# Kernel optimization log

Hardware: AMD Instinct MI355X
Metric: run time of the kernel (lower is better)

## Reference

```python
import jax, jax.numpy as jnp
import numpy as np

N, E, F, H, D, B = 50000, 800000, 128, 4, 32, 8  # nodes, edges, feat, heads, head_dim, graphs
NEG_SLOPE = 0.2


def _layer_norm(x, g, b, eps=1e-5):
    mu = jnp.mean(x, axis=-1, keepdims=True)
    var = jnp.var(x, axis=-1, keepdims=True)
    return (x - mu) * jax.lax.rsqrt(var + eps) * g + b


def _gat(x, src, dst, W, a_src, a_dst, bias):
    # PyG GATConv (eval): linear -> per-node alpha terms -> edge logits ->
    # per-destination segment softmax -> scatter-add weighted messages.
    h = (x @ W).reshape(N, H, D)                                  # [N,H,D]
    al_s = jnp.einsum('nhd,hd->nh', h, a_src)                     # [N,H]
    al_d = jnp.einsum('nhd,hd->nh', h, a_dst)                     # [N,H]
    logits = jax.nn.leaky_relu(al_s[src] + al_d[dst], NEG_SLOPE)  # [E+N,H]
    m = jax.ops.segment_max(logits, dst, num_segments=N)          # [N,H]
    ex = jnp.exp(logits - m[dst])
    denom = jax.ops.segment_sum(ex, dst, num_segments=N)          # [N,H]
    alpha = ex / denom[dst]                                       # [E+N,H]
    msg = h[src] * alpha[..., None]                               # [E+N,H,D]
    out = jax.ops.segment_sum(msg, dst, num_segments=N)           # [N,H,D]
    return out.reshape(N, H * D) + bias


def _gat_block(x, src, dst, W, a_src, a_dst, bias, ln_g, ln_b):
    out = _gat(x, src, dst, W, a_src, a_dst, bias)
    return _layer_norm(out + x, ln_g, ln_b)  # residual: dims match (128==128)


def setup_inputs() -> dict:
    key = jax.random.key(0)
    ks = jax.random.split(key, 24)
    s = 0.05
    inp = {
        'x': jax.random.normal(ks[0], (N, F), jnp.float32),
        'edge_index': jax.random.randint(ks[1], (2, E), 0, N, jnp.int32),
        'batch': jnp.sort(jax.random.randint(ks[2], (N,), 0, B, jnp.int32)),
    }
    i = 3
    for p in ('loc', 'reg'):
        inp[p + '_W'] = jax.random.normal(ks[i], (F, H * D)) * s; i += 1
        inp[p + '_att_src'] = jax.random.normal(ks[i], (H, D)) * s; i += 1
        inp[p + '_att_dst'] = jax.random.normal(ks[i], (H, D)) * s; i += 1
        inp[p + '_bias'] = jnp.zeros((H * D,))
        inp[p + '_ln_g'] = jnp.ones((F,))
        inp[p + '_ln_b'] = jnp.zeros((F,))
    inp['gp_W1'] = jax.random.normal(ks[i], (F, F)) * s; i += 1
    inp['gp_b1'] = jnp.zeros((F,))
    inp['gp_W2'] = jax.random.normal(ks[i], (F, F)) * s; i += 1
    inp['gp_b2'] = jnp.zeros((F,))
    inp['fu_W1'] = jax.random.normal(ks[i], (3 * F, 2 * F)) * s; i += 1
    inp['fu_b1'] = jnp.zeros((2 * F,))
    inp['fu_W2'] = jax.random.normal(ks[i], (2 * F, F)) * s; i += 1
    inp['fu_b2'] = jnp.zeros((F,))
    inp['fu_ln_g'] = jnp.ones((F,))
    inp['fu_ln_b'] = jnp.zeros((F,))
    return inp


def reference(x, edge_index, batch,
              loc_W, loc_att_src, loc_att_dst, loc_bias, loc_ln_g, loc_ln_b,
              reg_W, reg_att_src, reg_att_dst, reg_bias, reg_ln_g, reg_ln_b,
              gp_W1, gp_b1, gp_W2, gp_b2,
              fu_W1, fu_b1, fu_W2, fu_b2, fu_ln_g, fu_ln_b):
    # add self-loops (PyG GATConv default add_self_loops=True)
    loops = jnp.arange(N, dtype=edge_index.dtype)
    src = jnp.concatenate([edge_index[0], loops])
    dst = jnp.concatenate([edge_index[1], loops])

    local = _gat_block(x, src, dst, loc_W, loc_att_src, loc_att_dst, loc_bias, loc_ln_g, loc_ln_b)
    regional = _gat_block(x, src, dst, reg_W, reg_att_src, reg_att_dst, reg_bias, reg_ln_g, reg_ln_b)

    # global mean pool per graph, broadcast back to nodes
    sums = jax.ops.segment_sum(x, batch, num_segments=B)                  # [B,F]
    cnts = jax.ops.segment_sum(jnp.ones((N, 1), x.dtype), batch, num_segments=B)
    gctx = (sums / cnts)[batch]                                           # [N,F]
    gfeat = jax.nn.relu(gctx @ gp_W1 + gp_b1) @ gp_W2 + gp_b2

    cat = jnp.concatenate([local, regional, gfeat], axis=-1)              # [N,3F]
    fused = jax.nn.relu(cat @ fu_W1 + fu_b1) @ fu_W2 + fu_b2
    return _layer_norm(fused, fu_ln_g, fu_ln_b)
```

## Files before the change

kernel.cpp:

```cpp
#include <hip/hip_runtime.h>

#define NN 50000
#define EE 800000
#define FF 128
#define HH 4
#define BB 8
#define NEG 0.2f
#define NBLK ((NN + 255) / 256)

typedef __attribute__((ext_vector_type(8))) short s8v;
typedef __attribute__((ext_vector_type(4))) float f4v;

__device__ __forceinline__ unsigned short f2b(float f) {
    union { float f; unsigned u; } v; v.f = f;
    unsigned r = v.u + 0x7fffu + ((v.u >> 16) & 1u);
    return (unsigned short)(r >> 16);
}
__device__ __forceinline__ float b2f(unsigned short h) {
    union { unsigned u; float f; } v; v.u = ((unsigned)h) << 16;
    return v.f;
}
__device__ __forceinline__ float uasf(unsigned u) {
    union { unsigned u; float f; } v; v.u = u; return v.f;
}
__device__ __forceinline__ float lrelu(float t) { return t > 0.f ? t : NEG * t; }
__device__ __forceinline__ s8v cvt8(const float* p) {
    float4 f0 = *(const float4*)p;
    float4 f1 = *(const float4*)(p + 4);
    unsigned short u[8] = { f2b(f0.x), f2b(f0.y), f2b(f0.z), f2b(f0.w),
                            f2b(f1.x), f2b(f1.y), f2b(f1.z), f2b(f1.w) };
    return *(const s8v*)u;
}

__global__ void k_prep(const float* __restrict__ locW, const float* __restrict__ regW,
                       const float* __restrict__ W1, const float* __restrict__ W2,
                       unsigned short* __restrict__ Wt, unsigned short* __restrict__ W1t,
                       unsigned short* __restrict__ W2t, int* cur, float* pooled) {
    int i = blockIdx.x * 256 + threadIdx.x;
    if (i < 32768) {
        int n = i >> 7, k = i & 127;
        float v = n < 128 ? locW[k * 128 + n] : regW[k * 128 + n - 128];
        Wt[i] = f2b(v);
    } else if (i < 131072) {
        int j = i - 32768; int n = j / 384, k = j - n * 384;
        W1t[j] = f2b(W1[k * 256 + n]);
    } else if (i < 163840) {
        int j = i - 131072; int n = j >> 8, k = j & 255;
        W2t[j] = f2b(W2[k * 128 + n]);
    } else {
        int j = i - 163840;
        if (j < NN) cur[j] = 1;
        if (j < BB * FF) pooled[j] = 0.f;
    }
}

__global__ void k_count(const int* __restrict__ ei, int* cur) {
    int i = blockIdx.x * 256 + threadIdx.x;
    if (i < EE) atomicAdd(&cur[ei[EE + i]], 1);
}

__global__ __launch_bounds__(256) void k_scanA(int* cur, int* row_ptr, int* bsum) {
    __shared__ int wsum[4];
    int b = blockIdx.x, t = threadIdx.x;
    int i = b * 256 + t;
    int v = (i < NN) ? cur[i] : 0;
    if (i < NN) cur[i] = 0;
    int lane = t & 63, w = t >> 6;
    int sc = v;
#pragma unroll
    for (int off = 1; off < 64; off <<= 1) {
        int n = __shfl_up(sc, off);
        if (lane >= off) sc += n;
    }
    if (lane == 63) wsum[w] = sc;
    __syncthreads();
    int woff = 0;
    for (int k = 0; k < w; k++) woff += wsum[k];
    int incl = sc + woff;
    if (i < NN) row_ptr[i + 1] = incl;
    if (t == 255) bsum[b] = incl;
    if (i == 0) row_ptr[0] = 0;
}

__global__ __launch_bounds__(256) void k_scanC(int* row_ptr, const int* __restrict__ bsum) {
    __shared__ int ssum[4];
    int b = blockIdx.x, t = threadIdx.x;
    int lane = t & 63, w = t >> 6;
    int v = (t < b) ? bsum[t] : 0;
#pragma unroll
    for (int off = 32; off; off >>= 1) v += __shfl_xor(v, off);
    if (lane == 0) ssum[w] = v;
    __syncthreads();
    int off = ssum[0] + ssum[1] + ssum[2] + ssum[3];
    int i = b * 256 + t;
    if (i < NN && b > 0) row_ptr[i + 1] += off;
}

__global__ void k_scatter(const int* __restrict__ ei, const int* __restrict__ row_ptr,
                          int* cur, int* col) {
    int i = blockIdx.x * 256 + threadIdx.x;
    if (i < EE) {
        int s = ei[i], d = ei[EE + i];
        int p = atomicAdd(&cur[d], 1);
        col[row_ptr[d] + p] = s;
    } else if (i < EE + NN) {
        int n = i - EE;
        int p = atomicAdd(&cur[n], 1);
        col[row_ptr[n] + p] = n;
    }
}

__global__ __launch_bounds__(256) void k_gemm1(
    const float* __restrict__ x, const int* __restrict__ batch,
    const unsigned short* __restrict__ Wt,
    const float* __restrict__ loc_as, const float* __restrict__ loc_ad,
    const float* __restrict__ reg_as, const float* __restrict__ reg_ad,
    unsigned short* __restrict__ hl, unsigned short* __restrict__ hr,
    float* __restrict__ alc_s, float* __restrict__ alc_d,
    float* __restrict__ pooled) {
    __shared__ __align__(16) unsigned short SA[2][2048];
    __shared__ __align__(16) unsigned short SB[2][8192];
    __shared__ __align__(16) unsigned short Hs[16384];
    int t = threadIdx.x;
    int w = t >> 6, l = t & 63;
    int lq = l >> 4, lr = l & 15;
    int r0 = blockIdx.x * 64;

    int srow = t >> 2, sg = t & 3;
    int snode = r0 + srow; if (snode >= NN) snode = NN - 1;
    const float* xrow = x + (size_t)snode * 128 + sg * 8;

    f4v acc[4][4];
#pragma unroll
    for (int a0 = 0; a0 < 4; a0++)
#pragma unroll
        for (int b0 = 0; b0 < 4; b0++) acc[a0][b0] = (f4v){0.f, 0.f, 0.f, 0.f};

    *(s8v*)&SA[0][(sg * 64 + srow) * 8] = cvt8(xrow);
#pragma unroll
    for (int it = 0; it < 4; ++it) {
        int c = t + it * 256;
        int g = c & 3, n = c >> 2;
        *(s8v*)&SB[0][(g * 256 + n) * 8] = *(const s8v*)&Wt[(size_t)n * 128 + g * 8];
    }
    __syncthreads();
#pragma unroll
    for (int ks = 0; ks < 4; ++ks) {
        int cur = ks & 1;
        s8v pa; s8v pb[4];
        if (ks < 3) {
            pa = cvt8(xrow + (ks + 1) * 32);
#pragma unroll
            for (int it = 0; it < 4; ++it) {
                int c = t + it * 256;
                int g = c & 3, n = c >> 2;
                pb[it] = *(const s8v*)&Wt[(size_t)n * 128 + (ks + 1) * 32 + g * 8];
            }
        }
        s8v af[4], bf[4];
#pragma unroll
        for (int rf = 0; rf < 4; ++rf) af[rf] = *(const s8v*)&SA[cur][(lq * 64 + rf * 16 + lr) * 8];
#pragma unroll
        for (int cf = 0; cf < 4; ++cf) bf[cf] = *(const s8v*)&SB[cur][(lq * 256 + w * 64 + cf * 16 + lr) * 8];
#pragma unroll
        for (int rf = 0; rf < 4; ++rf)
#pragma unroll
            for (int cf = 0; cf < 4; ++cf)
                acc[rf][cf] = __builtin_amdgcn_mfma_f32_16x16x32_bf16(af[rf], bf[cf], acc[rf][cf], 0, 0, 0);
        if (ks < 3) {
            *(s8v*)&SA[cur ^ 1][(sg * 64 + srow) * 8] = pa;
#pragma unroll
            for (int it = 0; it < 4; ++it) {
                int c = t + it * 256;
                int g = c & 3, n = c >> 2;
                *(s8v*)&SB[cur ^ 1][(g * 256 + n) * 8] = pb[it];
            }
        }
        __syncthreads();
    }
#pragma unroll
    for (int cf = 0; cf < 4; ++cf) {
        int c = w * 64 + cf * 16 + lr;
#pragma unroll
        for (int rf = 0; rf < 4; ++rf)
#pragma unroll
            for (int i = 0; i < 4; ++i) {
                int row = rf * 16 + lq * 4 + i;
                Hs[((c >> 3) * 64 + row) * 8 + (c & 7)] = f2b(acc[rf][cf][i]);
            }
    }
    __syncthreads();
#pragma unroll
    for (int it = 0; it < 8; ++it) {
        int c = t + it * 256;
        int row = c >> 5, g = c & 31;
        int node = r0 + row;
        if (node < NN) {
            s8v v = *(const s8v*)&Hs[(g * 64 + row) * 8];
            int cc = g * 8;
            if (cc < 128) *(s8v*)&hl[(size_t)node * 128 + cc] = v;
            else          *(s8v*)&hr[(size_t)node * 128 + cc - 128] = v;
        }
    }
#pragma unroll
    for (int it = 0; it < 4; ++it) {
        int row = it * 16 + (t >> 4);
        int node = r0 + row;
        int q = t & 15;
        int gat = q >> 3, sd = (q >> 2) & 1, head = q & 3;
        const float* av = gat ? (sd ? reg_ad : reg_as) : (sd ? loc_ad : loc_as);
        float s = 0.f;
        int cbase = gat * 128 + head * 32;
        for (int d = 0; d < 32; ++d) {
            int c = cbase + d;
            s += b2f(Hs[((c >> 3) * 64 + row) * 8 + (c & 7)]) * av[head * 32 + d];
        }
        if (node < NN) {
            float* outp = sd ? alc_d : alc_s;
            outp[(size_t)node * 8 + gat * 4 + head] = s;
        }
    }
    {
        int colp = t & 127, halfp = t >> 7;
        int rbase = r0 + halfp * 32;
        int lastrow = r0 + 63; if (lastrow >= NN) lastrow = NN - 1;
        int blo = batch[r0 < NN ? r0 : NN - 1];
        int bhi = batch[lastrow];
        float acc0 = 0.f, acc1 = 0.f;
        for (int r = 0; r < 32; ++r) {
            int row = rbase + r;
            if (row < NN) {
                float v = x[(size_t)row * 128 + colp];
                int b = batch[row];
                if (b == blo) acc0 += v; else acc1 += v;
            }
        }
        atomicAdd(&pooled[blo * 128 + colp], acc0);
        if (bhi != blo) atomicAdd(&pooled[bhi * 128 + colp], acc1);
    }
}

__global__ __launch_bounds__(256) void k_gfeat8(
    const float* __restrict__ pooled, const int* __restrict__ batch,
    const float* __restrict__ W1, const float* __restrict__ b1,
    const float* __restrict__ W2, const float* __restrict__ b2,
    unsigned short* __restrict__ g8b) {
    __shared__ float mean_s[128];
    __shared__ float hid_s[128];
    __shared__ float part[256];
    __shared__ int bnd[2];
    int b = blockIdx.x, t = threadIdx.x;
    if (t < 2) {
        int target = b + t;
        int lo = 0, hi = NN;
        while (lo < hi) { int mid = (lo + hi) >> 1; if (batch[mid] < target) lo = mid + 1; else hi = mid; }
        bnd[t] = lo;
    }
    __syncthreads();
    int cnt = bnd[1] - bnd[0];
    float inv = cnt ? 1.f / (float)cnt : 0.f;
    if (t < 128) mean_s[t] = pooled[b * 128 + t] * inv;
    __syncthreads();
    int c = t & 127, kh = t >> 7;
    float a = 0.f;
    for (int k = kh * 64; k < kh * 64 + 64; k++) a += mean_s[k] * W1[k * 128 + c];
    part[t] = a;
    __syncthreads();
    if (t < 128) hid_s[t] = fmaxf(part[t] + part[t + 128] + b1[t], 0.f);
    __syncthreads();
    float a2 = 0.f;
    for (int k = kh * 64; k < kh * 64 + 64; k++) a2 += hid_s[k] * W2[k * 128 + c];
    part[t] = a2;
    __syncthreads();
    if (t < 128) g8b[b * 128 + t] = f2b(part[t] + part[t + 128] + b2[t]);
}

__global__ __launch_bounds__(256) void k_gat(
    const int* __restrict__ row_ptr, const int* __restrict__ col,
    const unsigned short* __restrict__ hl, const unsigned short* __restrict__ hr,
    const float* __restrict__ alc_s, const float* __restrict__ alc_d,
    const float* __restrict__ x,
    const float* __restrict__ loc_bias, const float* __restrict__ loc_g, const float* __restrict__ loc_b,
    const float* __restrict__ reg_bias, const float* __restrict__ reg_g, const float* __restrict__ reg_b,
    unsigned short* __restrict__ out_local, unsigned short* __restrict__ out_reg) {
    __shared__ float exA[4][64][4];
    __shared__ float exB[4][64][4];
    __shared__ int   colb[4][64];
    __shared__ int   degs[4];
    int w = threadIdx.x >> 6, lane = threadIdx.x & 63;
    int hA = lane >> 4;
    int node = blockIdx.x * 4 + w;
    int rp0 = row_ptr[node];
    int deg = row_ptr[node + 1] - rp0;
    if (lane == 0) degs[w] = deg;
    float4 adL = *(const float4*)&alc_d[(size_t)node * 8];
    float4 adR = *(const float4*)&alc_d[(size_t)node * 8 + 4];
    __syncthreads();
    int maxdeg = max(max(degs[0], degs[1]), max(degs[2], degs[3]));
    int chunks = (maxdeg + 63) >> 6;

    float sL0 = 0.f, sL1 = 0.f, sL2 = 0.f, sL3 = 0.f;
    float sR0 = 0.f, sR1 = 0.f, sR2 = 0.f, sR3 = 0.f;
    for (int base = 0; base < deg; base += 64) {
        int i = base + lane;
        bool v = i < deg;
        int s = col[rp0 + (v ? i : deg - 1)];
        float4 aL = *(const float4*)&alc_s[(size_t)s * 8];
        float4 aR = *(const float4*)&alc_s[(size_t)s * 8 + 4];
        float e0 = __expf(lrelu(aL.x + adL.x));
        float e1 = __expf(lrelu(aL.y + adL.y));
        float e2 = __expf(lrelu(aL.z + adL.z));
        float e3 = __expf(lrelu(aL.w + adL.w));
        float f0 = __expf(lrelu(aR.x + adR.x));
        float f1 = __expf(lrelu(aR.y + adR.y));
        float f2 = __expf(lrelu(aR.z + adR.z));
        float f3 = __expf(lrelu(aR.w + adR.w));
        if (!v) { e0 = e1 = e2 = e3 = f0 = f1 = f2 = f3 = 0.f; }
        *(float4*)&exA[w][lane][0] = make_float4(e0, e1, e2, e3);
        *(float4*)&exB[w][lane][0] = make_float4(f0, f1, f2, f3);
        colb[w][lane] = s;
        sL0 += e0; sL1 += e1; sL2 += e2; sL3 += e3;
        sR0 += f0; sR1 += f1; sR2 += f2; sR3 += f3;
    }
    __syncthreads();
#pragma unroll
    for (int off = 32; off; off >>= 1) {
        sL0 += __shfl_xor(sL0, off); sL1 += __shfl_xor(sL1, off);
        sL2 += __shfl_xor(sL2, off); sL3 += __shfl_xor(sL3, off);
        sR0 += __shfl_xor(sR0, off); sR1 += __shfl_xor(sR1, off);
        sR2 += __shfl_xor(sR2, off); sR3 += __shfl_xor(sR3, off);
    }
    float iA = (hA & 2) ? ((hA & 1) ? 1.f / sL3 : 1.f / sL2)
                        : ((hA & 1) ? 1.f / sL1 : 1.f / sL0);
    float iB = (hA & 2) ? ((hA & 1) ? 1.f / sR3 : 1.f / sR2)
                        : ((hA & 1) ? 1.f / sR1 : 1.f / sR0);

    float a0 = 0.f, a1 = 0.f, b0 = 0.f, b1 = 0.f;
    const unsigned* hlp = (const unsigned*)hl;
    const unsigned* hrp = (const unsigned*)hr;
    if (chunks == 1) {
#pragma unroll 4
        for (int e = 0; e < deg; ++e) {
            int s = colb[w][e];
            float eAv = exA[w][e][hA];
            float eBv = exB[w][e][hA];
            unsigned ul = hlp[(size_t)s * 64 + lane];
            unsigned ur = hrp[(size_t)s * 64 + lane];
            a0 += eAv * uasf(ul << 16);
            a1 += eAv * uasf(ul & 0xffff0000u);
            b0 += eBv * uasf(ur << 16);
            b1 += eBv * uasf(ur & 0xffff0000u);
        }
    } else {
        for (int c = 0; c < chunks; ++c) {
            int base = c * 64, i = base + lane;
            if (i < deg) {
                int s = col[rp0 + i];
                float4 aL = *(const float4*)&alc_s[(size_t)s * 8];
                float4 aR = *(const float4*)&alc_s[(size_t)s * 8 + 4];
                *(float4*)&exA[w][lane][0] = make_float4(
                    __expf(lrelu(aL.x + adL.x)), __expf(lrelu(aL.y + adL.y)),
                    __expf(lrelu(aL.z + adL.z)), __expf(lrelu(aL.w + adL.w)));
                *(float4*)&exB[w][lane][0] = make_float4(
                    __expf(lrelu(aR.x + adR.x)), __expf(lrelu(aR.y + adR.y)),
                    __expf(lrelu(aR.z + adR.z)), __expf(lrelu(aR.w + adR.w)));
                colb[w][lane] = s;
            }
            __syncthreads();
            int nc = deg - base; nc = nc < 0 ? 0 : (nc > 64 ? 64 : nc);
#pragma unroll 4
            for (int e = 0; e < nc; ++e) {
                int s = colb[w][e];
                float eAv = exA[w][e][hA];
                float eBv = exB[w][e][hA];
                unsigned ul = hlp[(size_t)s * 64 + lane];
                unsigned ur = hrp[(size_t)s * 64 + lane];
                a0 += eAv * uasf(ul << 16);
                a1 += eAv * uasf(ul & 0xffff0000u);
                b0 += eBv * uasf(ur << 16);
                b1 += eBv * uasf(ur & 0xffff0000u);
            }
            __syncthreads();
        }
    }

    int f = 2 * lane;
    float2 xr = *(const float2*)&x[(size_t)node * 128 + f];
    float2 lbi = *(const float2*)&loc_bias[f];
    float2 rbi = *(const float2*)&reg_bias[f];
    float v0 = a0 * iA + lbi.x + xr.x;
    float v1 = a1 * iA + lbi.y + xr.y;
    float u0 = b0 * iB + rbi.x + xr.x;
    float u1 = b1 * iB + rbi.y + xr.y;

    float sv = v0 + v1, su = u0 + u1;
#pragma unroll
    for (int off = 32; off; off >>= 1) { sv += __shfl_xor(sv, off); su += __shfl_xor(su, off); }
    float mv = sv * (1.f / 128.f), mu = su * (1.f / 128.f);
    float dv0 = v0 - mv, dv1 = v1 - mv, du0 = u0 - mu, du1 = u1 - mu;
    float qv = dv0 * dv0 + dv1 * dv1, qu = du0 * du0 + du1 * du1;
#pragma unroll
    for (int off = 32; off; off >>= 1) { qv += __shfl_xor(qv, off); qu += __shfl_xor(qu, off); }
    float rv = rsqrtf(qv * (1.f / 128.f) + 1e-5f), ru = rsqrtf(qu * (1.f / 128.f) + 1e-5f);
    float2 lg = *(const float2*)&loc_g[f], lb2 = *(const float2*)&loc_b[f];
    float2 rg = *(const float2*)&reg_g[f], rb2 = *(const float2*)&reg_b[f];
    unsigned pv = (unsigned)f2b(dv0 * rv * lg.x + lb2.x) | ((unsigned)f2b(dv1 * rv * lg.y + lb2.y) << 16);
    unsigned pu = (unsigned)f2b(du0 * ru * rg.x + rb2.x) | ((unsigned)f2b(du1 * ru * rg.y + rb2.y) << 16);
    *(unsigned*)&out_local[(size_t)node * 128 + f] = pv;
    *(unsigned*)&out_reg[(size_t)node * 128 + f]   = pu;
}

__global__ __launch_bounds__(256) void k_fusedm(
    const unsigned short* __restrict__ localb, const unsigned short* __restrict__ regionalb,
    const unsigned short* __restrict__ g8b, const int* __restrict__ batch,
    const unsigned short* __restrict__ W1t, const float* __restrict__ b1,
    const unsigned short* __restrict__ W2t, const float* __restrict__ b2,
    const float* __restrict__ lng, const float* __restrict__ lnb,
    float* __restrict__ out) {
    __shared__ __align__(16) unsigned short stg[20480];
    __shared__ __align__(16) unsigned short Hs[16384];
    unsigned short* SAb[2] = { stg, stg + 2048 };
    unsigned short* SBb[2] = { stg + 4096, stg + 12288 };
    unsigned short* W2Sb[2] = { stg, stg + 4096 };
    int t = threadIdx.x;
    int w = t >> 6, l = t & 63;
    int lq = l >> 4, lr = l & 15;
    int r0 = blockIdx.x * 64;

    int srow = t >> 2, sg = t & 3;
    int snode = r0 + srow; if (snode >= NN) snode = NN - 1;
    int sbatch = batch[snode];

    auto asrc = [&](int ks) -> const unsigned short* {
        int seg = ks >> 2;
        int ko = (ks & 3) * 32 + sg * 8;
        return seg == 0 ? localb + (size_t)snode * 128 + ko :
               seg == 1 ? regionalb + (size_t)snode * 128 + ko :
                          g8b + (size_t)sbatch * 128 + ko;
    };

    f4v acc[4][4];
#pragma unroll
    for (int a0 = 0; a0 < 4; a0++)
#pragma unroll
        for (int b0 = 0; b0 < 4; b0++) acc[a0][b0] = (f4v){0.f, 0.f, 0.f, 0.f};

    *(s8v*)&SAb[0][(sg * 64 + srow) * 8] = *(const s8v*)asrc(0);
#pragma unroll
    for (int it = 0; it < 4; ++it) {
        int c = t + it * 256;
        int g = c & 3, n = c >> 2;
        *(s8v*)&SBb[0][(g * 256 + n) * 8] = *(const s8v*)&W1t[(size_t)n * 384 + g * 8];
    }
    __syncthreads();
#pragma unroll
    for (int ks = 0; ks < 12; ++ks) {
        int cur = ks & 1;
        s8v pa; s8v pb[4];
        if (ks < 11) {
            pa = *(const s8v*)asrc(ks + 1);
#pragma unroll
            for (int it = 0; it < 4; ++it) {
                int c = t + it * 256;
                int g = c & 3, n = c >> 2;
                pb[it] = *(const s8v*)&W1t[(size_t)n * 384 + (ks + 1) * 32 + g * 8];
            }
        }
        s8v af[4], bf[4];
#pragma unroll
        for (int rf = 0; rf < 4; ++rf) af[rf] = *(const s8v*)&SAb[cur][(lq * 64 + rf * 16 + lr) * 8];
#pragma unroll
        for (int cf = 0; cf < 4; ++cf) bf[cf] = *(const s8v*)&SBb[cur][(lq * 256 + w * 64 + cf * 16 + lr) * 8];
#pragma unroll
        for (int rf = 0; rf < 4; ++rf)
#pragma unroll
            for (int cf = 0; cf < 4; ++cf)
                acc[rf][cf] = __builtin_amdgcn_mfma_f32_16x16x32_bf16(af[rf], bf[cf], acc[rf][cf], 0, 0, 0);
        if (ks < 11) {
            *(s8v*)&SAb[cur ^ 1][(sg * 64 + srow) * 8] = pa;
#pragma unroll
            for (int it = 0; it < 4; ++it) {
                int c = t + it * 256;
                int g = c & 3, n = c >> 2;
                *(s8v*)&SBb[cur ^ 1][(g * 256 + n) * 8] = pb[it];
            }
        }
        __syncthreads();
    }
#pragma unroll
    for (int cf = 0; cf < 4; ++cf) {
        int c = w * 64 + cf * 16 + lr;
        float bc = b1[c];
#pragma unroll
        for (int rf = 0; rf < 4; ++rf)
#pragma unroll
            for (int i = 0; i < 4; ++i) {
                int row = rf * 16 + lq * 4 + i;
                float v0 = acc[rf][cf][i] + bc;
                Hs[((c >> 3) * 64 + row) * 8 + (c & 7)] = f2b(v0 > 0.f ? v0 : 0.f);
            }
    }
    __syncthreads();
#pragma unroll
    for (int it = 0; it < 2; ++it) {
        int c = t + it * 256;
        int g = c & 3, n = c >> 2;
        *(s8v*)&W2Sb[0][(g * 128 + n) * 8] = *(const s8v*)&W2t[(size_t)n * 256 + g * 8];
    }
    __syncthreads();
    f4v a2[8];
#pragma unroll
    for (int cf = 0; cf < 8; ++cf) a2[cf] = (f4v){0.f, 0.f, 0.f, 0.f};
#pragma unroll
    for (int ks = 0; ks < 8; ++ks) {
        int cur = ks & 1;
        s8v pw[2];
        if (ks < 7) {
#pragma unroll
            for (int it = 0; it < 2; ++it) {
                int c = t + it * 256;
                int g = c & 3, n = c >> 2;
                pw[it] = *(const s8v*)&W2t[(size_t)n * 256 + (ks + 1) * 32 + g * 8];
            }
        }
        s8v af = *(const s8v*)&Hs[((ks * 4 + lq) * 64 + w * 16 + lr) * 8];
#pragma unroll
        for (int cf = 0; cf < 8; ++cf) {
            s8v bfv = *(const s8v*)&W2Sb[cur][(lq * 128 + cf * 16 + lr) * 8];
            a2[cf] = __builtin_amdgcn_mfma_f32_16x16x32_bf16(af, bfv, a2[cf], 0, 0, 0);
        }
        if (ks < 7) {
#pragma unroll
            for (int it = 0; it < 2; ++it) {
                int c = t + it * 256;
                int g = c & 3, n = c >> 2;
                *(s8v*)&W2Sb[cur ^ 1][(g * 128 + n) * 8] = pw[it];
            }
        }
        __syncthreads();
    }
    float b2c[8], gc[8], bc2[8];
#pragma unroll
    for (int cf = 0; cf < 8; ++cf) {
        int c = cf * 16 + lr;
        b2c[cf] = b2[c]; gc[cf] = lng[c]; bc2[cf] = lnb[c];
    }
#pragma unroll
    for (int i = 0; i < 4; ++i) {
        int row = w * 16 + lq * 4 + i;
        int node = r0 + row;
        float vals[8]; float s = 0.f;
#pragma unroll
        for (int cf = 0; cf < 8; ++cf) { vals[cf] = a2[cf][i] + b2c[cf]; s += vals[cf]; }
        s += __shfl_xor(s, 1); s += __shfl_xor(s, 2); s += __shfl_xor(s, 4); s += __shfl_xor(s, 8);
        float mean = s * (1.f / 128.f);
        float vs = 0.f;
#pragma unroll
        for (int cf = 0; cf < 8; ++cf) { float d = vals[cf] - mean; vs += d * d; }
        vs += __shfl_xor(vs, 1); vs += __shfl_xor(vs, 2); vs += __shfl_xor(vs, 4); vs += __shfl_xor(vs, 8);
        float rstd = rsqrtf(vs * (1.f / 128.f) + 1e-5f);
        if (node < NN) {
#pragma unroll
            for (int cf = 0; cf < 8; ++cf)
                out[(size_t)node * 128 + cf * 16 + lr] = (vals[cf] - mean) * rstd * gc[cf] + bc2[cf];
        }
    }
}

extern "C" void kernel_launch(void* const* d_in, const int* in_sizes, int n_in,
                              void* d_out, int out_size, void* d_ws, size_t ws_size,
                              hipStream_t stream) {
    const float* x      = (const float*)d_in[0];
    const int*   ei     = (const int*)d_in[1];
    const int*   batch  = (const int*)d_in[2];
    const float* locW   = (const float*)d_in[3];
    const float* loc_as = (const float*)d_in[4];
    const float* loc_ad = (const float*)d_in[5];
    const float* loc_bi = (const float*)d_in[6];
    const float* loc_g  = (const float*)d_in[7];
    const float* loc_b  = (const float*)d_in[8];
    const float* regW   = (const float*)d_in[9];
    const float* reg_as = (const float*)d_in[10];
    const float* reg_ad = (const float*)d_in[11];
    const float* reg_bi = (const float*)d_in[12];
    const float* reg_g  = (const float*)d_in[13];
    const float* reg_b  = (const float*)d_in[14];
    const float* gp_W1  = (const float*)d_in[15];
    const float* gp_b1  = (const float*)d_in[16];
    const float* gp_W2  = (const float*)d_in[17];
    const float* gp_b2  = (const float*)d_in[18];
    const float* fu_W1  = (const float*)d_in[19];
    const float* fu_b1  = (const float*)d_in[20];
    const float* fu_W2  = (const float*)d_in[21];
    const float* fu_b2  = (const float*)d_in[22];
    const float* fu_lg  = (const float*)d_in[23];
    const float* fu_lb  = (const float*)d_in[24];
    float* out = (float*)d_out;

    char* ws = (char*)d_ws;
    size_t off = 0;
    auto alloc = [&](size_t bytes) { void* p = ws + off; off += (bytes + 255) & ~(size_t)255; return p; };
    unsigned short* hl        = (unsigned short*)alloc((size_t)NN * 128 * 2);
    unsigned short* hr        = (unsigned short*)alloc((size_t)NN * 128 * 2);
    unsigned short* localb    = (unsigned short*)alloc((size_t)NN * 128 * 2);
    unsigned short* regionalb = (unsigned short*)alloc((size_t)NN * 128 * 2);
    float* alc_s  = (float*)alloc((size_t)NN * 8 * 4);
    float* alc_d  = (float*)alloc((size_t)NN * 8 * 4);
    int* row_ptr  = (int*)alloc((size_t)(NN + 1) * 4);
    int* cur      = (int*)alloc((size_t)NN * 4);
    int* col      = (int*)alloc((size_t)(EE + NN) * 4);
    float* pooled = (float*)alloc((size_t)BB * 128 * 4);
    unsigned short* g8b = (unsigned short*)alloc((size_t)BB * 128 * 2);
    unsigned short* Wt  = (unsigned short*)alloc((size_t)32768 * 2);
    unsigned short* W1t = (unsigned short*)alloc((size_t)98304 * 2);
    unsigned short* W2t = (unsigned short*)alloc((size_t)32768 * 2);
    int* bsum = (int*)alloc((size_t)NBLK * 4);

    hipLaunchKernelGGL(k_prep, dim3(640 + NBLK), dim3(256), 0, stream,
                       locW, regW, fu_W1, fu_W2, Wt, W1t, W2t, cur, pooled);
    hipLaunchKernelGGL(k_count, dim3((EE + 255) / 256), dim3(256), 0, stream, ei, cur);
    hipLaunchKernelGGL(k_scanA, dim3(NBLK), dim3(256), 0, stream, cur, row_ptr, bsum);
    hipLaunchKernelGGL(k_scanC, dim3(NBLK), dim3(256), 0, stream, row_ptr, bsum);
    hipLaunchKernelGGL(k_scatter, dim3((EE + NN + 255) / 256), dim3(256), 0, stream, ei, row_ptr, cur, col);
    hipLaunchKernelGGL(k_gemm1, dim3((NN + 63) / 64), dim3(256), 0, stream,
                       x, batch, Wt, loc_as, loc_ad, reg_as, reg_ad,
                       hl, hr, alc_s, alc_d, pooled);
    hipLaunchKernelGGL(k_gfeat8, dim3(BB), dim3(256), 0, stream,
                       pooled, batch, gp_W1, gp_b1, gp_W2, gp_b2, g8b);
    hipLaunchKernelGGL(k_gat, dim3(NN / 4), dim3(256), 0, stream,
                       row_ptr, col, hl, hr, alc_s, alc_d, x,
                       loc_bi, loc_g, loc_b, reg_bi, reg_g, reg_b,
                       localb, regionalb);
    hipLaunchKernelGGL(k_fusedm, dim3((NN + 63) / 64), dim3(256), 0, stream,
                       localb, regionalb, g8b, batch,
                       W1t, fu_b1, W2t, fu_b2, fu_lg, fu_lb, out);
}
```

Baseline: 273.1 us.

## Precompute per-graph global-feature projection and place self-loops at segment ends

The global-context slice of the fusion MLP's first layer is identical for every node in a graph, so its product with the corresponding rows of fu_W1 is now computed once per graph in k_gfeat8 and added as a bias in k_fusedm. This removes a third of the K loop in the fused GEMM. Separately, self-loop entries are written directly at the last slot of each CSR row in k_scanC, so k_scatter no longer does atomics for them. Self-loops are always last in each row, and the fusion contribution of the global features now stays in fp32 instead of going through bf16.

```diff
diff --git a/kernel.cpp b/kernel.cpp
--- a/kernel.cpp
+++ b/kernel.cpp
@@ -82,7 +82,8 @@
     if (i == 0) row_ptr[0] = 0;
 }
 
-__global__ __launch_bounds__(256) void k_scanC(int* row_ptr, const int* __restrict__ bsum) {
+__global__ __launch_bounds__(256) void k_scanC(int* row_ptr, const int* __restrict__ bsum,
+                                               int* __restrict__ col) {
     __shared__ int ssum[4];
     int b = blockIdx.x, t = threadIdx.x;
     int lane = t & 63, w = t >> 6;
@@ -93,7 +94,11 @@
     __syncthreads();
     int off = ssum[0] + ssum[1] + ssum[2] + ssum[3];
     int i = b * 256 + t;
-    if (i < NN && b > 0) row_ptr[i + 1] += off;
+    if (i < NN) {
+        int fin = row_ptr[i + 1] + (b > 0 ? off : 0);
+        if (b > 0) row_ptr[i + 1] = fin;
+        col[fin - 1] = i;
+    }
 }
 
 __global__ void k_scatter(const int* __restrict__ ei, const int* __restrict__ row_ptr,
@@ -103,10 +108,6 @@
         int s = ei[i], d = ei[EE + i];
         int p = atomicAdd(&cur[d], 1);
         col[row_ptr[d] + p] = s;
-    } else if (i < EE + NN) {
-        int n = i - EE;
-        int p = atomicAdd(&cur[n], 1);
-        col[row_ptr[n] + p] = n;
     }
 }
 
@@ -244,10 +245,12 @@
     const float* __restrict__ pooled, const int* __restrict__ batch,
     const float* __restrict__ W1, const float* __restrict__ b1,
     const float* __restrict__ W2, const float* __restrict__ b2,
-    unsigned short* __restrict__ g8b) {
+    const float* __restrict__ fuW1,
+    float* __restrict__ gpre) {
     __shared__ float mean_s[128];
     __shared__ float hid_s[128];
     __shared__ float part[256];
+    __shared__ float g8s[128];
     __shared__ int bnd[2];
     int b = blockIdx.x, t = threadIdx.x;
     if (t < 2) {
@@ -272,7 +275,11 @@
     for (int k = kh * 64; k < kh * 64 + 64; k++) a2 += hid_s[k] * W2[k * 128 + c];
     part[t] = a2;
     __syncthreads();
-    if (t < 128) g8b[b * 128 + t] = f2b(part[t] + part[t + 128] + b2[t]);
+    if (t < 128) g8s[t] = part[t] + part[t + 128] + b2[t];
+    __syncthreads();
+    float a3 = 0.f;
+    for (int k = 0; k < 128; k++) a3 += g8s[k] * fuW1[(size_t)(256 + k) * 256 + t];
+    gpre[(size_t)b * 256 + t] = a3;
 }
 
 __global__ __launch_bounds__(256) void k_gat(
@@ -412,13 +419,14 @@
 
 __global__ __launch_bounds__(256) void k_fusedm(
     const unsigned short* __restrict__ localb, const unsigned short* __restrict__ regionalb,
-    const unsigned short* __restrict__ g8b, const int* __restrict__ batch,
+    const float* __restrict__ gpre, const int* __restrict__ batch,
     const unsigned short* __restrict__ W1t, const float* __restrict__ b1,
     const unsigned short* __restrict__ W2t, const float* __restrict__ b2,
     const float* __restrict__ lng, const float* __restrict__ lnb,
     float* __restrict__ out) {
     __shared__ __align__(16) unsigned short stg[20480];
     __shared__ __align__(16) unsigned short Hs[16384];
+    __shared__ int bS[64];
     unsigned short* SAb[2] = { stg, stg + 2048 };
     unsigned short* SBb[2] = { stg + 4096, stg + 12288 };
     unsigned short* W2Sb[2] = { stg, stg + 4096 };
@@ -429,14 +437,16 @@
 
     int srow = t >> 2, sg = t & 3;
     int snode = r0 + srow; if (snode >= NN) snode = NN - 1;
-    int sbatch = batch[snode];
+    if (t < 64) {
+        int n = r0 + t; if (n >= NN) n = NN - 1;
+        bS[t] = batch[n];
+    }
 
     auto asrc = [&](int ks) -> const unsigned short* {
         int seg = ks >> 2;
         int ko = (ks & 3) * 32 + sg * 8;
         return seg == 0 ? localb + (size_t)snode * 128 + ko :
-               seg == 1 ? regionalb + (size_t)snode * 128 + ko :
-                          g8b + (size_t)sbatch * 128 + ko;
+                          regionalb + (size_t)snode * 128 + ko;
     };
 
     f4v acc[4][4];
@@ -454,10 +464,10 @@
     }
     __syncthreads();
 #pragma unroll
-    for (int ks = 0; ks < 12; ++ks) {
+    for (int ks = 0; ks < 8; ++ks) {
         int cur = ks & 1;
         s8v pa; s8v pb[4];
-        if (ks < 11) {
+        if (ks < 7) {
             pa = *(const s8v*)asrc(ks + 1);
 #pragma unroll
             for (int it = 0; it < 4; ++it) {
@@ -476,7 +486,7 @@
 #pragma unroll
             for (int cf = 0; cf < 4; ++cf)
                 acc[rf][cf] = __builtin_amdgcn_mfma_f32_16x16x32_bf16(af[rf], bf[cf], acc[rf][cf], 0, 0, 0);
-        if (ks < 11) {
+        if (ks < 7) {
             *(s8v*)&SAb[cur ^ 1][(sg * 64 + srow) * 8] = pa;
 #pragma unroll
             for (int it = 0; it < 4; ++it) {
@@ -496,7 +506,7 @@
 #pragma unroll
             for (int i = 0; i < 4; ++i) {
                 int row = rf * 16 + lq * 4 + i;
-                float v0 = acc[rf][cf][i] + bc;
+                float v0 = acc[rf][cf][i] + bc + gpre[(size_t)bS[row] * 256 + c];
                 Hs[((c >> 3) * 64 + row) * 8 + (c & 7)] = f2b(v0 > 0.f ? v0 : 0.f);
             }
     }
@@ -610,7 +620,7 @@
     int* cur      = (int*)alloc((size_t)NN * 4);
     int* col      = (int*)alloc((size_t)(EE + NN) * 4);
     float* pooled = (float*)alloc((size_t)BB * 128 * 4);
-    unsigned short* g8b = (unsigned short*)alloc((size_t)BB * 128 * 2);
+    float* gpre   = (float*)alloc((size_t)BB * 256 * 4);
     unsigned short* Wt  = (unsigned short*)alloc((size_t)32768 * 2);
     unsigned short* W1t = (unsigned short*)alloc((size_t)98304 * 2);
     unsigned short* W2t = (unsigned short*)alloc((size_t)32768 * 2);
@@ -620,18 +630,18 @@
                        locW, regW, fu_W1, fu_W2, Wt, W1t, W2t, cur, pooled);
     hipLaunchKernelGGL(k_count, dim3((EE + 255) / 256), dim3(256), 0, stream, ei, cur);
     hipLaunchKernelGGL(k_scanA, dim3(NBLK), dim3(256), 0, stream, cur, row_ptr, bsum);
-    hipLaunchKernelGGL(k_scanC, dim3(NBLK), dim3(256), 0, stream, row_ptr, bsum);
-    hipLaunchKernelGGL(k_scatter, dim3((EE + NN + 255) / 256), dim3(256), 0, stream, ei, row_ptr, cur, col);
+    hipLaunchKernelGGL(k_scanC, dim3(NBLK), dim3(256), 0, stream, row_ptr, bsum, col);
+    hipLaunchKernelGGL(k_scatter, dim3((EE + 255) / 256), dim3(256), 0, stream, ei, row_ptr, cur, col);
     hipLaunchKernelGGL(k_gemm1, dim3((NN + 63) / 64), dim3(256), 0, stream,
                        x, batch, Wt, loc_as, loc_ad, reg_as, reg_ad,
                        hl, hr, alc_s, alc_d, pooled);
     hipLaunchKernelGGL(k_gfeat8, dim3(BB), dim3(256), 0, stream,
-                       pooled, batch, gp_W1, gp_b1, gp_W2, gp_b2, g8b);
+                       pooled, batch, gp_W1, gp_b1, gp_W2, gp_b2, fu_W1, gpre);
     hipLaunchKernelGGL(k_gat, dim3(NN / 4), dim3(256), 0, stream,
                        row_ptr, col, hl, hr, alc_s, alc_d, x,
                        loc_bi, loc_g, loc_b, reg_bi, reg_g, reg_b,
                        localb, regionalb);
     hipLaunchKernelGGL(k_fusedm, dim3((NN + 63) / 64), dim3(256), 0, stream,
-                       localb, regionalb, g8b, batch,
+                       localb, regionalb, gpre, batch,
                        W1t, fu_b1, W2t, fu_b2, fu_lg, fu_lb, out);
 }
```

After: 276.3 us. No clear change (+1.2%).
